# Kernel tuning notes

Measured on AMD Instinct MI355X. Metric: run time of the kernel, lower is better.

The kernel has to match this reference:

```python
import jax, jax.numpy as jnp
import numpy as np

N = 50000
E = 1000000
FN = 16
FE = 8
H = 64
DH = 64
LN_EPS = 1e-5


def _layernorm(x, g, b):
    mu = jnp.mean(x, axis=-1, keepdims=True)
    var = jnp.var(x, axis=-1, keepdims=True)
    return (x - mu) * jax.lax.rsqrt(var + LN_EPS) * g + b


def setup_inputs() -> dict:
    key = jax.random.key(0)
    ks = jax.random.split(key, 24)

    def w(k, i, o):
        return jax.random.normal(k, (i, o), jnp.float32) / np.sqrt(i).astype(np.float32)

    inp = {}
    inp["x"] = jax.random.normal(ks[0], (N, FN), jnp.float32)
    inp["edge_index"] = jax.random.randint(ks[1], (2, E), 0, N, dtype=jnp.int32)
    inp["edge_attr"] = jax.random.normal(ks[2], (E, FE), jnp.float32)
    # layer 0 (in_dim = FN, residual is a Linear since FN != H)
    inp["l0_lin_w"] = w(ks[3], FE, FN); inp["l0_lin_b"] = jnp.zeros((FN,), jnp.float32)
    inp["l0_w1"] = w(ks[4], FN, H);    inp["l0_b1"] = jnp.zeros((H,), jnp.float32)
    inp["l0_w2"] = w(ks[5], H, H);     inp["l0_b2"] = jnp.zeros((H,), jnp.float32)
    inp["l0_ln_g"] = jnp.ones((H,), jnp.float32); inp["l0_ln_b"] = jnp.zeros((H,), jnp.float32)
    inp["l0_res_w"] = w(ks[6], FN, H); inp["l0_res_b"] = jnp.zeros((H,), jnp.float32)
    # layers 1, 2 (in_dim = H, residual = identity)
    for li, base in ((1, 7), (2, 11)):
        inp[f"l{li}_lin_w"] = w(ks[base], FE, H);   inp[f"l{li}_lin_b"] = jnp.zeros((H,), jnp.float32)
        inp[f"l{li}_w1"] = w(ks[base + 1], H, H);   inp[f"l{li}_b1"] = jnp.zeros((H,), jnp.float32)
        inp[f"l{li}_w2"] = w(ks[base + 2], H, H);   inp[f"l{li}_b2"] = jnp.zeros((H,), jnp.float32)
        inp[f"l{li}_ln_g"] = jnp.ones((H,), jnp.float32)
        inp[f"l{li}_ln_b"] = jnp.zeros((H,), jnp.float32)
    D_IN = 4 * H + FE
    inp["dec_w1"] = w(ks[20], D_IN, DH);    inp["dec_b1"] = jnp.zeros((DH,), jnp.float32)
    inp["dec_w2"] = w(ks[21], DH, DH // 2); inp["dec_b2"] = jnp.zeros((DH // 2,), jnp.float32)
    inp["dec_w3"] = w(ks[22], DH // 2, 1);  inp["dec_b3"] = jnp.zeros((1,), jnp.float32)
    return inp


def _block(x, src, dst, edge_attr, lin_w, lin_b, w1, b1, w2, b2, ln_g, ln_b, res):
    # GINEConv: message = ReLU(x_src + Lin(edge_attr)); sum-aggregate at dst; eps=0
    msg = jax.nn.relu(x[src] + edge_attr @ lin_w + lin_b)      # (E, D_in)
    aggr = jax.ops.segment_sum(msg, dst, num_segments=N)       # (N, D_in)
    h = jax.nn.relu((x + aggr) @ w1 + b1) @ w2 + b2            # GIN nn MLP -> (N, H)
    h = jax.nn.relu(h)                                         # dropout inactive (eval)
    return _layernorm(h + res, ln_g, ln_b)


def reference(x, edge_index, edge_attr,
              l0_lin_w, l0_lin_b, l0_w1, l0_b1, l0_w2, l0_b2, l0_ln_g, l0_ln_b, l0_res_w, l0_res_b,
              l1_lin_w, l1_lin_b, l1_w1, l1_b1, l1_w2, l1_b2, l1_ln_g, l1_ln_b,
              l2_lin_w, l2_lin_b, l2_w1, l2_b1, l2_w2, l2_b2, l2_ln_g, l2_ln_b,
              dec_w1, dec_b1, dec_w2, dec_b2, dec_w3, dec_b3):
    src, dst = edge_index[0], edge_index[1]
    h = _block(x, src, dst, edge_attr, l0_lin_w, l0_lin_b, l0_w1, l0_b1, l0_w2, l0_b2,
               l0_ln_g, l0_ln_b, x @ l0_res_w + l0_res_b)
    h = _block(h, src, dst, edge_attr, l1_lin_w, l1_lin_b, l1_w1, l1_b1, l1_w2, l1_b2,
               l1_ln_g, l1_ln_b, h)
    h = _block(h, src, dst, edge_attr, l2_lin_w, l2_lin_b, l2_w1, l2_b1, l2_w2, l2_b2,
               l2_ln_g, l2_ln_b, h)
    hs, hd = h[src], h[dst]                                    # (E, H) each
    z = jnp.concatenate([hs, hd, jnp.abs(hs - hd), hs * hd, edge_attr], axis=-1)  # (E, 4H+FE)
    z = jax.nn.relu(z @ dec_w1 + dec_b1)
    z = jax.nn.relu(z @ dec_w2 + dec_b2)
    return (z @ dec_w3 + dec_b3)[:, 0]                         # (E,)
```

## Files before the change

kernel.cpp:

```cpp
#include <hip/hip_runtime.h>

#define NN 50000
#define NE 1000000

constexpr float LN_EPS = 1e-5f;

typedef short bf16x8 __attribute__((ext_vector_type(8)));
typedef float f32x4 __attribute__((ext_vector_type(4)));
typedef uint uvec4 __attribute__((ext_vector_type(4)));
typedef uint uvec2 __attribute__((ext_vector_type(2)));

__device__ inline uint cvtpk(float a, float b) {
  uint r;
  asm("v_cvt_pk_bf16_f32 %0, %1, %2" : "=v"(r) : "v"(a), "v"(b));
  return r;
}
__device__ inline ushort cvt1(float a) {
  uint r;
  asm("v_cvt_pk_bf16_f32 %0, %1, %1" : "=v"(r) : "v"(a));
  return (ushort)r;
}
__device__ inline float bflo(uint u) { union { uint x; float f; } v; v.x = u << 16; return v.f; }
__device__ inline float bfhi(uint u) { union { uint x; float f; } v; v.x = u & 0xffff0000u; return v.f; }

__global__ __launch_bounds__(256) void hist_kernel(const int* __restrict__ ei,
                                                   int* __restrict__ cnt) {
  int e = blockIdx.x * 256 + threadIdx.x;
  if (e < NE) atomicAdd(&cnt[ei[NE + e]], 1);
}

__global__ __launch_bounds__(256) void scan1_kernel(const int* __restrict__ cnt,
                                                    int* __restrict__ off,
                                                    int* __restrict__ bsum) {
  __shared__ int sh[256];
  int t = threadIdx.x;
  int idx = blockIdx.x * 256 + t;
  int v = (idx < NN) ? cnt[idx] : 0;
  sh[t] = v;
  __syncthreads();
  for (int o = 1; o < 256; o <<= 1) {
    int xv = (t >= o) ? sh[t - o] : 0;
    __syncthreads();
    sh[t] += xv;
    __syncthreads();
  }
  if (idx <= NN) off[idx] = sh[t] - v;
  if (t == 255) bsum[blockIdx.x] = sh[255];
}

__global__ __launch_bounds__(256) void scan2_kernel(int* __restrict__ bsum, int nb) {
  __shared__ int sh[256];
  int t = threadIdx.x;
  int v = (t < nb) ? bsum[t] : 0;
  sh[t] = v;
  __syncthreads();
  for (int o = 1; o < 256; o <<= 1) {
    int xv = (t >= o) ? sh[t - o] : 0;
    __syncthreads();
    sh[t] += xv;
    __syncthreads();
  }
  if (t < nb) bsum[t] = sh[t] - v;
}

__global__ __launch_bounds__(256) void scan3_kernel(int* __restrict__ off,
                                                    const int* __restrict__ bsum,
                                                    int* __restrict__ cnt) {
  int idx = blockIdx.x * 256 + threadIdx.x;
  if (idx <= NN) off[idx] += bsum[blockIdx.x];
  if (idx < NN) cnt[idx] = 0;
}

__global__ __launch_bounds__(256) void scatter_kernel(
    const int* __restrict__ ei, const float* __restrict__ ea,
    const int* __restrict__ off, int* __restrict__ cur,
    int* __restrict__ ipos, int* __restrict__ srcp, int* __restrict__ dstp,
    ushort* __restrict__ eapb) {
  int e = blockIdx.x * 256 + threadIdx.x;
  if (e < NE) {
    int d = ei[NE + e];
    int s = ei[e];
    int p = off[d] + atomicAdd(&cur[d], 1);
    ipos[e] = p;
    srcp[p] = s;
    dstp[p] = d;
    const float* eaf = ea + (size_t)e * 8;
    f32x4 e0 = *(const f32x4*)(eaf);
    f32x4 e1 = *(const f32x4*)(eaf + 4);
    uvec4 u;
    u.x = cvtpk(e0.x, e0.y);
    u.y = cvtpk(e0.z, e0.w);
    u.z = cvtpk(e1.x, e1.y);
    u.w = cvtpk(e1.z, e1.w);
    __builtin_nontemporal_store(u, (uvec4*)(eapb + (size_t)p * 8));
  }
}

__global__ __launch_bounds__(256) void unperm_kernel(const float* __restrict__ tmp,
                                                     const int* __restrict__ ipos,
                                                     float* __restrict__ out) {
  int e = blockIdx.x * 256 + threadIdx.x;
  if (e < NE) out[e] = tmp[ipos[e]];
}

__device__ inline float lane_layernorm(float r, float g, float b) {
  float s = r;
#pragma unroll
  for (int m = 32; m >= 1; m >>= 1) s += __shfl_xor(s, m);
  float mu = s * (1.f / 64.f);
  float dv = r - mu;
  float v = dv * dv;
#pragma unroll
  for (int m = 32; m >= 1; m >>= 1) v += __shfl_xor(v, m);
  float var = v * (1.f / 64.f);
  return dv * rsqrtf(var + LN_EPS) * g + b;
}

__global__ __launch_bounds__(256) void layer0_fused(
    const float* __restrict__ x, float* __restrict__ hout,
    ushort* __restrict__ houtbf,
    const ushort* __restrict__ eapb, const int* __restrict__ srcp,
    const int* __restrict__ off,
    const float* __restrict__ lw, const float* __restrict__ lb,
    const float* __restrict__ w1, const float* __restrict__ b1,
    const float* __restrict__ w2, const float* __restrict__ b2,
    const float* __restrict__ lng, const float* __restrict__ lnb,
    const float* __restrict__ rw, const float* __restrict__ rb) {
  int n = blockIdx.x * 4 + (threadIdx.x >> 6);
  int j = threadIdx.x & 63;
  int d = j & 15, slot = j >> 4;
  int start = off[n], end = off[n + 1];
  float lwv[8];
#pragma unroll
  for (int i = 0; i < 8; i++) lwv[i] = lw[i * 16 + d];
  float lbv = lb[d];
  float acc = 0.f;
  for (int base = start; base < end; base += 64) {
    int idx = base + j;
    int sl = (idx < end) ? srcp[idx] : 0;
    int c = min(end - base, 64);
    for (int i0 = 0; i0 < c; i0 += 4) {
      int i = i0 + slot;
      bool valid = i < c;
      int ii = i & 63;
      int s = __shfl(sl, ii);
      int pp = min(base + i0 + slot, NE - 1);
      float ev = bflo((uint)eapb[(size_t)pp * 8 + (d & 7)]);
      float xs = x[(size_t)s * 16 + d];
      float m = lbv + xs;
#pragma unroll
      for (int q = 0; q < 8; q++) m = fmaf(__shfl(ev, slot * 16 + q), lwv[q], m);
      m = fmaxf(m, 0.f);
      acc += valid ? m : 0.f;
    }
  }
  acc += __shfl_xor(acc, 16);
  acc += __shfl_xor(acc, 32);
  float xr = x[(size_t)n * 16 + d];
  float t = xr + acc;
  float q1 = b1[j];
#pragma unroll 4
  for (int k = 0; k < 16; k++) q1 = fmaf(__shfl(t, k), w1[k * 64 + j], q1);
  q1 = fmaxf(q1, 0.f);
  float h2 = b2[j];
  for (int k = 0; k < 64; k++) h2 = fmaf(__shfl(q1, k), w2[k * 64 + j], h2);
  h2 = fmaxf(h2, 0.f);
  float res = rb[j];
#pragma unroll 4
  for (int k = 0; k < 16; k++) res = fmaf(__shfl(xr, k), rw[k * 64 + j], res);
  float v = lane_layernorm(h2 + res, lng[j], lnb[j]);
  hout[(size_t)n * 64 + j] = v;
  houtbf[(size_t)n * 64 + j] = cvt1(v);
}

__device__ inline float edge8_msg(const ushort* __restrict__ hinb, int s, int j,
                                  uint ulo, uint uhi, uint vlo, uint vhi,
                                  const float* lwv, float lbv) {
  float hc = bflo((uint)hinb[(size_t)s * 64 + j]);
  float m = lbv + hc;
  m = fmaf(bflo(ulo), lwv[0], m);
  m = fmaf(bfhi(ulo), lwv[1], m);
  m = fmaf(bflo(uhi), lwv[2], m);
  m = fmaf(bfhi(uhi), lwv[3], m);
  m = fmaf(bflo(vlo), lwv[4], m);
  m = fmaf(bfhi(vlo), lwv[5], m);
  m = fmaf(bflo(vhi), lwv[6], m);
  m = fmaf(bfhi(vhi), lwv[7], m);
  return fmaxf(m, 0.f);
}

__global__ __launch_bounds__(256) void aggr_kernel(
    const ushort* __restrict__ hinb, float* __restrict__ tout,
    const ushort* __restrict__ eapb, const int* __restrict__ srcp,
    const int* __restrict__ off,
    const float* __restrict__ lw, const float* __restrict__ lb) {
  int n = blockIdx.x * 4 + (threadIdx.x >> 6);
  int j = threadIdx.x & 63;
  int start = __builtin_amdgcn_readfirstlane(off[n]);
  int end = __builtin_amdgcn_readfirstlane(off[n + 1]);
  float lwv[8];
#pragma unroll
  for (int i = 0; i < 8; i++) lwv[i] = lw[i * 64 + j];
  float lbv = lb[j];
  float acc = 0.f;
  int p = start;
  for (; p + 8 <= end; p += 8) {
    const uvec4* ip = (const uvec4*)(srcp + p);
    uvec4 I0 = __builtin_nontemporal_load(ip + 0);
    uvec4 I1 = __builtin_nontemporal_load(ip + 1);
    int s0 = __builtin_amdgcn_readfirstlane((int)I0.x);
    int s1 = __builtin_amdgcn_readfirstlane((int)I0.y);
    int s2 = __builtin_amdgcn_readfirstlane((int)I0.z);
    int s3 = __builtin_amdgcn_readfirstlane((int)I0.w);
    int s4 = __builtin_amdgcn_readfirstlane((int)I1.x);
    int s5 = __builtin_amdgcn_readfirstlane((int)I1.y);
    int s6 = __builtin_amdgcn_readfirstlane((int)I1.z);
    int s7 = __builtin_amdgcn_readfirstlane((int)I1.w);
    const uvec4* ep = (const uvec4*)(eapb + (size_t)p * 8);
    uint ua[8][4];
#pragma unroll
    for (int i = 0; i < 8; i++) {
      uvec4 E = __builtin_nontemporal_load(ep + i);
      ua[i][0] = __builtin_amdgcn_readfirstlane(E.x);
      ua[i][1] = __builtin_amdgcn_readfirstlane(E.y);
      ua[i][2] = __builtin_amdgcn_readfirstlane(E.z);
      ua[i][3] = __builtin_amdgcn_readfirstlane(E.w);
    }
    acc += edge8_msg(hinb, s0, j, ua[0][0], ua[0][1], ua[0][2], ua[0][3], lwv, lbv);
    acc += edge8_msg(hinb, s1, j, ua[1][0], ua[1][1], ua[1][2], ua[1][3], lwv, lbv);
    acc += edge8_msg(hinb, s2, j, ua[2][0], ua[2][1], ua[2][2], ua[2][3], lwv, lbv);
    acc += edge8_msg(hinb, s3, j, ua[3][0], ua[3][1], ua[3][2], ua[3][3], lwv, lbv);
    acc += edge8_msg(hinb, s4, j, ua[4][0], ua[4][1], ua[4][2], ua[4][3], lwv, lbv);
    acc += edge8_msg(hinb, s5, j, ua[5][0], ua[5][1], ua[5][2], ua[5][3], lwv, lbv);
    acc += edge8_msg(hinb, s6, j, ua[6][0], ua[6][1], ua[6][2], ua[6][3], lwv, lbv);
    acc += edge8_msg(hinb, s7, j, ua[7][0], ua[7][1], ua[7][2], ua[7][3], lwv, lbv);
  }
  for (; p < end; p++) {
    int s = __builtin_amdgcn_readfirstlane(srcp[p]);
    uvec4 E = __builtin_nontemporal_load((const uvec4*)(eapb + (size_t)p * 8));
    uint e0 = __builtin_amdgcn_readfirstlane(E.x);
    uint e1 = __builtin_amdgcn_readfirstlane(E.y);
    uint e2 = __builtin_amdgcn_readfirstlane(E.z);
    uint e3 = __builtin_amdgcn_readfirstlane(E.w);
    acc += edge8_msg(hinb, s, j, e0, e1, e2, e3, lwv, lbv);
  }
  tout[(size_t)n * 64 + j] = acc;
}

__global__ __launch_bounds__(256) void prep_kernel(
    const float* __restrict__ w1, const float* __restrict__ w2,
    ushort* __restrict__ w1f, ushort* __restrict__ w2f) {
  int t = blockIdx.x * 256 + threadIdx.x;
  if (t < 18432) {
    int j = t & 7, lane = (t >> 3) & 63, f = t >> 9;
    int k = (f >> 2) * 32 + ((lane >> 4) * 8) + j;
    int n = (f & 3) * 16 + (lane & 15);
    float v = (k < 264) ? w1[k * 64 + n] : 0.f;
    w1f[t] = cvt1(v);
  } else {
    int t2 = t - 18432;
    int j = t2 & 7, lane = (t2 >> 3) & 63, f = t2 >> 9;
    int k = (f >> 1) * 32 + ((lane >> 4) * 8) + j;
    int n = (f & 1) * 16 + (lane & 15);
    w2f[t2] = cvt1(w2[k * 32 + n]);
  }
}

__global__ __launch_bounds__(256) void prep_mlpw(
    const float* __restrict__ w1a, const float* __restrict__ w2a,
    const float* __restrict__ w1b, const float* __restrict__ w2b,
    ushort* __restrict__ out) {
  int t = blockIdx.x * 256 + threadIdx.x;
  int layer = t >> 13, wsel = (t >> 12) & 1, idx = t & 4095;
  const float* w = layer ? (wsel ? w2b : w1b) : (wsel ? w2a : w1a);
  int j = idx & 7, lane = (idx >> 3) & 63, f = idx >> 9;
  int k = (f >> 2) * 32 + ((lane >> 4) * 8) + j;
  int n = (f & 3) * 16 + (lane & 15);
  float v = w[k * 64 + n];
  ushort h = cvt1(v);
  float r = v - bflo((uint)h);
  ushort lo = cvt1(r);
  int base = layer * 16384 + wsel * 8192;
  out[base + idx] = h;
  out[base + 4096 + idx] = lo;
}

#define YS2 68

__global__ __launch_bounds__(128) void mlp_kernel(
    const float* __restrict__ tacc, const float* __restrict__ hinf,
    float* __restrict__ houtf, ushort* __restrict__ houtbf,
    const ushort* __restrict__ wf,
    const float* __restrict__ b1, const float* __restrict__ b2,
    const float* __restrict__ lng, const float* __restrict__ lnb) {
  __shared__ float ybuf[2][32 * YS2];
  const int w = threadIdx.x >> 6, l = threadIdx.x & 63;
  const int sub = l & 15, quad = l >> 4;
  const int wid = blockIdx.x * 2 + w;
  const int r0 = wid * 32;
  if (r0 >= NN) return;
  float* Y = ybuf[w];

  const bf16x8* w1h = (const bf16x8*)wf;
  const bf16x8* w1l = (const bf16x8*)(wf + 4096);
  const bf16x8* w2h = (const bf16x8*)(wf + 8192);
  const bf16x8* w2l = (const bf16x8*)(wf + 12288);

  union UF { uvec4 u; bf16x8 v; };

  bf16x8 Ahi[2][2], Alo[2][2];
#pragma unroll
  for (int m = 0; m < 2; m++) {
    int row = min(r0 + m * 16 + sub, NN - 1);
    const float* pt = tacc + (size_t)row * 64 + quad * 8;
    const float* ph = hinf + (size_t)row * 64 + quad * 8;
#pragma unroll
    for (int ks = 0; ks < 2; ks++) {
      f32x4 t0 = *(const f32x4*)(pt + ks * 32);
      f32x4 t1 = *(const f32x4*)(pt + ks * 32 + 4);
      f32x4 h0 = *(const f32x4*)(ph + ks * 32);
      f32x4 h1 = *(const f32x4*)(ph + ks * 32 + 4);
      t0 += h0;
      t1 += h1;
      UF uh, ul;
      uh.u.x = cvtpk(t0.x, t0.y);
      uh.u.y = cvtpk(t0.z, t0.w);
      uh.u.z = cvtpk(t1.x, t1.y);
      uh.u.w = cvtpk(t1.z, t1.w);
      ul.u.x = cvtpk(t0.x - bflo(uh.u.x), t0.y - bfhi(uh.u.x));
      ul.u.y = cvtpk(t0.z - bflo(uh.u.y), t0.w - bfhi(uh.u.y));
      ul.u.z = cvtpk(t1.x - bflo(uh.u.z), t1.y - bfhi(uh.u.z));
      ul.u.w = cvtpk(t1.z - bflo(uh.u.w), t1.w - bfhi(uh.u.w));
      Ahi[m][ks] = uh.v;
      Alo[m][ks] = ul.v;
    }
  }

  f32x4 c1[2][4];
#pragma unroll
  for (int m = 0; m < 2; m++)
#pragma unroll
    for (int nb = 0; nb < 4; nb++) c1[m][nb] = (f32x4){0.f, 0.f, 0.f, 0.f};
#pragma unroll
  for (int nb = 0; nb < 4; nb++) {
#pragma unroll
    for (int ks = 0; ks < 2; ks++) {
      bf16x8 bh = w1h[(ks * 4 + nb) * 64 + l];
      bf16x8 bl = w1l[(ks * 4 + nb) * 64 + l];
      c1[0][nb] = __builtin_amdgcn_mfma_f32_16x16x32_bf16(Ahi[0][ks], bh, c1[0][nb], 0, 0, 0);
      c1[1][nb] = __builtin_amdgcn_mfma_f32_16x16x32_bf16(Ahi[1][ks], bh, c1[1][nb], 0, 0, 0);
      c1[0][nb] = __builtin_amdgcn_mfma_f32_16x16x32_bf16(Alo[0][ks], bh, c1[0][nb], 0, 0, 0);
      c1[1][nb] = __builtin_amdgcn_mfma_f32_16x16x32_bf16(Alo[1][ks], bh, c1[1][nb], 0, 0, 0);
      c1[0][nb] = __builtin_amdgcn_mfma_f32_16x16x32_bf16(Ahi[0][ks], bl, c1[0][nb], 0, 0, 0);
      c1[1][nb] = __builtin_amdgcn_mfma_f32_16x16x32_bf16(Ahi[1][ks], bl, c1[1][nb], 0, 0, 0);
    }
  }

  float b1v[4];
#pragma unroll
  for (int nb = 0; nb < 4; nb++) b1v[nb] = b1[nb * 16 + sub];
#pragma unroll
  for (int m = 0; m < 2; m++)
#pragma unroll
    for (int nb = 0; nb < 4; nb++)
#pragma unroll
      for (int r = 0; r < 4; r++)
        Y[(m * 16 + quad * 4 + r) * YS2 + nb * 16 + sub] =
            fmaxf(c1[m][nb][r] + b1v[nb], 0.f);

  bf16x8 Qhi[2][2], Qlo[2][2];
#pragma unroll
  for (int m = 0; m < 2; m++) {
#pragma unroll
    for (int ks = 0; ks < 2; ks++) {
      const float* py = &Y[(m * 16 + sub) * YS2 + ks * 32 + quad * 8];
      f32x4 q0 = *(const f32x4*)py;
      f32x4 q1 = *(const f32x4*)(py + 4);
      UF uh, ul;
      uh.u.x = cvtpk(q0.x, q0.y);
      uh.u.y = cvtpk(q0.z, q0.w);
      uh.u.z = cvtpk(q1.x, q1.y);
      uh.u.w = cvtpk(q1.z, q1.w);
      ul.u.x = cvtpk(q0.x - bflo(uh.u.x), q0.y - bfhi(uh.u.x));
      ul.u.y = cvtpk(q0.z - bflo(uh.u.y), q0.w - bfhi(uh.u.y));
      ul.u.z = cvtpk(q1.x - bflo(uh.u.z), q1.y - bfhi(uh.u.z));
      ul.u.w = cvtpk(q1.z - bflo(uh.u.w), q1.w - bfhi(uh.u.w));
      Qhi[m][ks] = uh.v;
      Qlo[m][ks] = ul.v;
    }
  }

  f32x4 c2[2][4];
#pragma unroll
  for (int m = 0; m < 2; m++)
#pragma unroll
    for (int nb = 0; nb < 4; nb++) c2[m][nb] = (f32x4){0.f, 0.f, 0.f, 0.f};
#pragma unroll
  for (int nb = 0; nb < 4; nb++) {
#pragma unroll
    for (int ks = 0; ks < 2; ks++) {
      bf16x8 bh = w2h[(ks * 4 + nb) * 64 + l];
      bf16x8 bl = w2l[(ks * 4 + nb) * 64 + l];
      c2[0][nb] = __builtin_amdgcn_mfma_f32_16x16x32_bf16(Qhi[0][ks], bh, c2[0][nb], 0, 0, 0);
      c2[1][nb] = __builtin_amdgcn_mfma_f32_16x16x32_bf16(Qhi[1][ks], bh, c2[1][nb], 0, 0, 0);
      c2[0][nb] = __builtin_amdgcn_mfma_f32_16x16x32_bf16(Qlo[0][ks], bh, c2[0][nb], 0, 0, 0);
      c2[1][nb] = __builtin_amdgcn_mfma_f32_16x16x32_bf16(Qlo[1][ks], bh, c2[1][nb], 0, 0, 0);
      c2[0][nb] = __builtin_amdgcn_mfma_f32_16x16x32_bf16(Qhi[0][ks], bl, c2[0][nb], 0, 0, 0);
      c2[1][nb] = __builtin_amdgcn_mfma_f32_16x16x32_bf16(Qhi[1][ks], bl, c2[1][nb], 0, 0, 0);
    }
  }

  float b2v[4], lngv[4], lnbv[4];
#pragma unroll
  for (int nb = 0; nb < 4; nb++) {
    b2v[nb] = b2[nb * 16 + sub];
    lngv[nb] = lng[nb * 16 + sub];
    lnbv[nb] = lnb[nb * 16 + sub];
  }
#pragma unroll
  for (int m = 0; m < 2; m++) {
#pragma unroll
    for (int r = 0; r < 4; r++) {
      int node = r0 + m * 16 + quad * 4 + r;
      int nc = min(node, NN - 1);
      float vp[4];
      float s = 0.f;
#pragma unroll
      for (int nb = 0; nb < 4; nb++) {
        vp[nb] = fmaxf(c2[m][nb][r] + b2v[nb], 0.f) +
                 hinf[(size_t)nc * 64 + nb * 16 + sub];
        s += vp[nb];
      }
      s += __shfl_xor(s, 1);
      s += __shfl_xor(s, 2);
      s += __shfl_xor(s, 4);
      s += __shfl_xor(s, 8);
      float mu = s * (1.f / 64.f);
      float vv = 0.f;
      float dv[4];
#pragma unroll
      for (int nb = 0; nb < 4; nb++) {
        dv[nb] = vp[nb] - mu;
        vv += dv[nb] * dv[nb];
      }
      vv += __shfl_xor(vv, 1);
      vv += __shfl_xor(vv, 2);
      vv += __shfl_xor(vv, 4);
      vv += __shfl_xor(vv, 8);
      float rstd = rsqrtf(vv * (1.f / 64.f) + LN_EPS);
      if (node < NN) {
#pragma unroll
        for (int nb = 0; nb < 4; nb++) {
          float o = dv[nb] * rstd * lngv[nb] + lnbv[nb];
          if (houtf) houtf[(size_t)node * 64 + nb * 16 + sub] = o;
          houtbf[(size_t)node * 64 + nb * 16 + sub] = cvt1(o);
        }
      }
    }
  }
}

#define YS 72
#define NBLK 15625
#define BPX 1954

__device__ inline void absmul(bf16x8 a, bf16x8 b, bf16x8& dd, bf16x8& pp) {
  union U { bf16x8 v; uvec4 u; } ua, ub, ud, up;
  ua.v = a; ub.v = b;
#pragma unroll
  for (int i = 0; i < 4; i++) {
    float a0 = bflo(ua.u[i]), a1 = bfhi(ua.u[i]);
    float b0 = bflo(ub.u[i]), b1 = bfhi(ub.u[i]);
    ud.u[i] = cvtpk(fabsf(a0 - b0), fabsf(a1 - b1));
    up.u[i] = cvtpk(a0 * b0, a1 * b1);
  }
  dd = ud.v; pp = up.v;
}

__global__ __launch_bounds__(128, 4) void decoder_kernel(
    const ushort* __restrict__ hb,
    const int* __restrict__ srcp, const int* __restrict__ dstp,
    const ushort* __restrict__ eapb,
    const ushort* __restrict__ w1f, const ushort* __restrict__ w2f,
    const float* __restrict__ b1, const float* __restrict__ b2,
    const float* __restrict__ w3, const float* __restrict__ b3,
    float* __restrict__ tmp) {
  __shared__ ushort ybuf[2][32 * YS];
  const int w = threadIdx.x >> 6, l = threadIdx.x & 63;
  const int sub = l & 15, quad = l >> 4;
  int bb = (blockIdx.x & 7) * BPX + (blockIdx.x >> 3);
  if (bb >= NBLK) return;
  const int g = bb * 2 + w;
  ushort* Y = ybuf[w];

  int s32 = __builtin_nontemporal_load(&srcp[g * 32 + (l & 31)]);
  int d32 = __builtin_nontemporal_load(&dstp[g * 32 + (l & 31)]);

  bf16x8 alo[2], ahi[2], blo[2], bhi[2];
#pragma unroll
  for (int m = 0; m < 2; m++) {
    int sA = __shfl(s32, m * 16 + sub);
    int dA = __shfl(d32, m * 16 + sub);
    const ushort* pa = hb + (size_t)sA * 64 + quad * 8;
    const ushort* pb = hb + (size_t)dA * 64 + quad * 8;
    alo[m] = *(const bf16x8*)pa;
    ahi[m] = *(const bf16x8*)(pa + 32);
    blo[m] = *(const bf16x8*)pb;
    bhi[m] = *(const bf16x8*)(pb + 32);
  }
  bf16x8 eaf0 = (bf16x8){0, 0, 0, 0, 0, 0, 0, 0};
  bf16x8 eaf1 = (bf16x8){0, 0, 0, 0, 0, 0, 0, 0};
  if (quad == 0) {
    eaf0 = *(const bf16x8*)&eapb[((size_t)g * 32 + sub) * 8];
    eaf1 = *(const bf16x8*)&eapb[((size_t)g * 32 + 16 + sub) * 8];
  }

  float b1v[4];
#pragma unroll
  for (int t = 0; t < 4; t++) b1v[t] = b1[t * 16 + sub];
  float b2v0 = b2[sub], b2v1 = b2[16 + sub];
  float w3v0 = w3[sub], w3v1 = w3[16 + sub];
  float b3v = b3[0];

  f32x4 acc[2][4];
#pragma unroll
  for (int m = 0; m < 2; m++)
#pragma unroll
    for (int t = 0; t < 4; t++) acc[m][t] = (f32x4){0.f, 0.f, 0.f, 0.f};

#define MF(sB, f0, f1)                                                        \
  {                                                                           \
    _Pragma("unroll") for (int t = 0; t < 4; t++) {                           \
      bf16x8 bfv = ((const bf16x8*)w1f)[((sB)*4 + t) * 64 + l];               \
      acc[0][t] = __builtin_amdgcn_mfma_f32_16x16x32_bf16(f0, bfv, acc[0][t], \
                                                          0, 0, 0);           \
      acc[1][t] = __builtin_amdgcn_mfma_f32_16x16x32_bf16(f1, bfv, acc[1][t], \
                                                          0, 0, 0);           \
    }                                                                         \
  }

  {
    bf16x8 dlo0, plo0, dlo1, plo1;
    absmul(alo[0], blo[0], dlo0, plo0);
    absmul(alo[1], blo[1], dlo1, plo1);
    MF(0, alo[0], alo[1]);
    MF(2, blo[0], blo[1]);
    MF(4, dlo0, dlo1);
    MF(6, plo0, plo1);
  }
  {
    bf16x8 dhi0, phi0, dhi1, phi1;
    absmul(ahi[0], bhi[0], dhi0, phi0);
    absmul(ahi[1], bhi[1], dhi1, phi1);
    MF(1, ahi[0], ahi[1]);
    MF(3, bhi[0], bhi[1]);
    MF(5, dhi0, dhi1);
    MF(7, phi0, phi1);
  }
  MF(8, eaf0, eaf1);
#undef MF

#pragma unroll
  for (int m = 0; m < 2; m++)
#pragma unroll
    for (int t = 0; t < 4; t++)
#pragma unroll
      for (int r = 0; r < 4; r++)
        Y[(m * 16 + quad * 4 + r) * YS + t * 16 + sub] =
            cvt1(fmaxf(acc[m][t][r] + b1v[t], 0.f));

  bf16x8 w2frag[4];
#pragma unroll
  for (int f = 0; f < 4; f++) w2frag[f] = ((const bf16x8*)w2f)[f * 64 + l];
  f32x4 acc2[2][2];
#pragma unroll
  for (int m = 0; m < 2; m++) {
    acc2[m][0] = (f32x4){0.f, 0.f, 0.f, 0.f};
    acc2[m][1] = (f32x4){0.f, 0.f, 0.f, 0.f};
#pragma unroll
    for (int ks = 0; ks < 2; ks++) {
      bf16x8 ya = *(const bf16x8*)&Y[(m * 16 + sub) * YS + ks * 32 + quad * 8];
      acc2[m][0] = __builtin_amdgcn_mfma_f32_16x16x32_bf16(ya, w2frag[ks * 2 + 0],
                                                           acc2[m][0], 0, 0, 0);
      acc2[m][1] = __builtin_amdgcn_mfma_f32_16x16x32_bf16(ya, w2frag[ks * 2 + 1],
                                                           acc2[m][1], 0, 0, 0);
    }
  }
#pragma unroll
  for (int m = 0; m < 2; m++)
#pragma unroll
    for (int r = 0; r < 4; r++) {
      float o = fmaxf(acc2[m][0][r] + b2v0, 0.f) * w3v0 +
                fmaxf(acc2[m][1][r] + b2v1, 0.f) * w3v1;
      o += __shfl_xor(o, 1);
      o += __shfl_xor(o, 2);
      o += __shfl_xor(o, 4);
      o += __shfl_xor(o, 8);
      if (sub == 0) tmp[g * 32 + m * 16 + quad * 4 + r] = o + b3v;
    }
}

extern "C" void kernel_launch(void* const* d_in, const int* in_sizes, int n_in,
                              void* d_out, int out_size, void* d_ws, size_t ws_size,
                              hipStream_t stream) {
  const float* x = (const float*)d_in[0];
  const int* ei = (const int*)d_in[1];
  const float* ea = (const float*)d_in[2];
  const float* l0_lin_w = (const float*)d_in[3];
  const float* l0_lin_b = (const float*)d_in[4];
  const float* l0_w1 = (const float*)d_in[5];
  const float* l0_b1 = (const float*)d_in[6];
  const float* l0_w2 = (const float*)d_in[7];
  const float* l0_b2 = (const float*)d_in[8];
  const float* l0_ln_g = (const float*)d_in[9];
  const float* l0_ln_b = (const float*)d_in[10];
  const float* l0_res_w = (const float*)d_in[11];
  const float* l0_res_b = (const float*)d_in[12];
  const float* dec_w1 = (const float*)d_in[29];
  const float* dec_b1 = (const float*)d_in[30];
  const float* dec_w2 = (const float*)d_in[31];
  const float* dec_b2 = (const float*)d_in[32];
  const float* dec_w3 = (const float*)d_in[33];
  const float* dec_b3 = (const float*)d_in[34];

  float* h_a = (float*)d_ws;
  float* h_b = h_a + (size_t)NN * 64;
  ushort* hbA = (ushort*)(h_b + (size_t)NN * 64);
  ushort* hbB = hbA + (size_t)NN * 64;
  int* ipos = (int*)(hbB + (size_t)NN * 64);
  int* srcp = ipos + NE;
  int* dstp = srcp + NE;
  float* tmp = (float*)(dstp + NE);
  int* off = (int*)(tmp + NE);
  int* cnt = off + (NN + 1);
  int* bsum = cnt + NN;
  ushort* w1f = (ushort*)(bsum + 256);
  ushort* w2f = w1f + 18432;
  ushort* eapb = w2f + 2048;
  ushort* wmlp = eapb + (size_t)NE * 8;
  float* tacc = (float*)(wmlp + 32768);

  const int EB = (NE + 255) / 256;
  const int SB = (NN + 256) / 256;
  const int MB = ((NN + 31) / 32 + 1) / 2;

  hipMemsetAsync(cnt, 0, (size_t)NN * sizeof(int), stream);
  hist_kernel<<<EB, 256, 0, stream>>>(ei, cnt);
  scan1_kernel<<<SB, 256, 0, stream>>>(cnt, off, bsum);
  scan2_kernel<<<1, 256, 0, stream>>>(bsum, SB);
  scan3_kernel<<<SB, 256, 0, stream>>>(off, bsum, cnt);
  scatter_kernel<<<EB, 256, 0, stream>>>(ei, ea, off, cnt, ipos, srcp, dstp, eapb);
  prep_mlpw<<<64, 256, 0, stream>>>((const float*)d_in[15], (const float*)d_in[17],
                                    (const float*)d_in[23], (const float*)d_in[25],
                                    wmlp);

  layer0_fused<<<NN / 4, 256, 0, stream>>>(x, h_a, hbA, eapb, srcp, off,
                                           l0_lin_w, l0_lin_b, l0_w1, l0_b1,
                                           l0_w2, l0_b2, l0_ln_g, l0_ln_b,
                                           l0_res_w, l0_res_b);
  aggr_kernel<<<NN / 4, 256, 0, stream>>>(hbA, tacc, eapb, srcp, off,
                                          (const float*)d_in[13],
                                          (const float*)d_in[14]);
  mlp_kernel<<<MB, 128, 0, stream>>>(tacc, h_a, h_b, hbB, wmlp,
                                     (const float*)d_in[16], (const float*)d_in[18],
                                     (const float*)d_in[19], (const float*)d_in[20]);
  aggr_kernel<<<NN / 4, 256, 0, stream>>>(hbB, tacc, eapb, srcp, off,
                                          (const float*)d_in[21],
                                          (const float*)d_in[22]);
  mlp_kernel<<<MB, 128, 0, stream>>>(tacc, h_b, (float*)nullptr, hbA, wmlp + 16384,
                                     (const float*)d_in[24], (const float*)d_in[26],
                                     (const float*)d_in[27], (const float*)d_in[28]);

  prep_kernel<<<80, 256, 0, stream>>>(dec_w1, dec_w2, w1f, w2f);
  decoder_kernel<<<8 * BPX, 128, 0, stream>>>(hbA, srcp, dstp, eapb,
                                              w1f, w2f, dec_b1, dec_b2,
                                              dec_w3, dec_b3, tmp);
  unperm_kernel<<<EB, 256, 0, stream>>>(tmp, ipos, (float*)d_out);
}
```

Before: 572.6 us.

## Split layer-0 into aggregation and MFMA-based node MLP kernels

The fused layer-0 kernel, which ran its node MLP with per-lane scalar FMA loops over shuffles, is split in two. An aggregation kernel now writes 16-wide aggregated sums, and a new mlp0 kernel computes W1, W2 and the residual projection with bf16 split-precision (hi/lo) MFMA plus layernorm, using pre-packed weights. This moves the dense per-node work off slow shuffle-FMA loops, at the cost of an extra launch and a round trip of the 16-wide sums through global memory.

```diff
diff --git a/kernel.cpp b/kernel.cpp
--- a/kernel.cpp
+++ b/kernel.cpp
@@ -103,29 +103,11 @@
   if (e < NE) out[e] = tmp[ipos[e]];
 }
 
-__device__ inline float lane_layernorm(float r, float g, float b) {
-  float s = r;
-#pragma unroll
-  for (int m = 32; m >= 1; m >>= 1) s += __shfl_xor(s, m);
-  float mu = s * (1.f / 64.f);
-  float dv = r - mu;
-  float v = dv * dv;
-#pragma unroll
-  for (int m = 32; m >= 1; m >>= 1) v += __shfl_xor(v, m);
-  float var = v * (1.f / 64.f);
-  return dv * rsqrtf(var + LN_EPS) * g + b;
-}
-
-__global__ __launch_bounds__(256) void layer0_fused(
-    const float* __restrict__ x, float* __restrict__ hout,
-    ushort* __restrict__ houtbf,
+__global__ __launch_bounds__(256) void aggr0_kernel(
+    const float* __restrict__ x, float* __restrict__ tout16,
     const ushort* __restrict__ eapb, const int* __restrict__ srcp,
     const int* __restrict__ off,
-    const float* __restrict__ lw, const float* __restrict__ lb,
-    const float* __restrict__ w1, const float* __restrict__ b1,
-    const float* __restrict__ w2, const float* __restrict__ b2,
-    const float* __restrict__ lng, const float* __restrict__ lnb,
-    const float* __restrict__ rw, const float* __restrict__ rb) {
+    const float* __restrict__ lw, const float* __restrict__ lb) {
   int n = blockIdx.x * 4 + (threadIdx.x >> 6);
   int j = threadIdx.x & 63;
   int d = j & 15, slot = j >> 4;
@@ -156,21 +138,7 @@
   }
   acc += __shfl_xor(acc, 16);
   acc += __shfl_xor(acc, 32);
-  float xr = x[(size_t)n * 16 + d];
-  float t = xr + acc;
-  float q1 = b1[j];
-#pragma unroll 4
-  for (int k = 0; k < 16; k++) q1 = fmaf(__shfl(t, k), w1[k * 64 + j], q1);
-  q1 = fmaxf(q1, 0.f);
-  float h2 = b2[j];
-  for (int k = 0; k < 64; k++) h2 = fmaf(__shfl(q1, k), w2[k * 64 + j], h2);
-  h2 = fmaxf(h2, 0.f);
-  float res = rb[j];
-#pragma unroll 4
-  for (int k = 0; k < 16; k++) res = fmaf(__shfl(xr, k), rw[k * 64 + j], res);
-  float v = lane_layernorm(h2 + res, lng[j], lnb[j]);
-  hout[(size_t)n * 64 + j] = v;
-  houtbf[(size_t)n * 64 + j] = cvt1(v);
+  if (slot == 0) tout16[(size_t)n * 16 + d] = acc;
 }
 
 __device__ inline float edge8_msg(const ushort* __restrict__ hinb, int s, int j,
@@ -285,6 +253,36 @@
   out[base + 4096 + idx] = lo;
 }
 
+__global__ __launch_bounds__(256) void prep_mlp0(
+    const float* __restrict__ w1, const float* __restrict__ w2,
+    const float* __restrict__ rw, ushort* __restrict__ out) {
+  int t = blockIdx.x * 256 + threadIdx.x;
+  if (t < 4096) {
+    int which = t >> 11, idx = t & 2047;
+    int j = idx & 7, lane = (idx >> 3) & 63, f = idx >> 9;
+    int k = ((lane >> 4) * 8) + j;
+    int n = f * 16 + (lane & 15);
+    float v;
+    if (which == 0) v = (k < 16) ? w1[k * 64 + n] : 0.f;
+    else            v = (k >= 16) ? rw[(k - 16) * 64 + n] : 0.f;
+    ushort h = cvt1(v);
+    float r = v - bflo((uint)h);
+    int base = which * 4096;
+    out[base + idx] = h;
+    out[base + 2048 + idx] = cvt1(r);
+  } else {
+    int idx = t - 4096;
+    int j = idx & 7, lane = (idx >> 3) & 63, f = idx >> 9;
+    int k = (f >> 2) * 32 + ((lane >> 4) * 8) + j;
+    int n = (f & 3) * 16 + (lane & 15);
+    float v = w2[k * 64 + n];
+    ushort h = cvt1(v);
+    float r = v - bflo((uint)h);
+    out[8192 + idx] = h;
+    out[12288 + idx] = cvt1(r);
+  }
+}
+
 #define YS2 68
 
 __global__ __launch_bounds__(128) void mlp_kernel(
@@ -453,6 +451,186 @@
         for (int nb = 0; nb < 4; nb++) {
           float o = dv[nb] * rstd * lngv[nb] + lnbv[nb];
           if (houtf) houtf[(size_t)node * 64 + nb * 16 + sub] = o;
+          houtbf[(size_t)node * 64 + nb * 16 + sub] = cvt1(o);
+        }
+      }
+    }
+  }
+}
+
+__global__ __launch_bounds__(128) void mlp0_kernel(
+    const float* __restrict__ x, const float* __restrict__ tacc16,
+    float* __restrict__ houtf, ushort* __restrict__ houtbf,
+    const ushort* __restrict__ wf,
+    const float* __restrict__ b1, const float* __restrict__ b2,
+    const float* __restrict__ rb,
+    const float* __restrict__ lng, const float* __restrict__ lnb) {
+  __shared__ float ybuf[2][32 * YS2];
+  const int w = threadIdx.x >> 6, l = threadIdx.x & 63;
+  const int sub = l & 15, quad = l >> 4;
+  const int wid = blockIdx.x * 2 + w;
+  const int r0 = wid * 32;
+  if (r0 >= NN) return;
+  float* Y = ybuf[w];
+
+  const bf16x8* B1h = (const bf16x8*)wf;
+  const bf16x8* B1l = (const bf16x8*)(wf + 2048);
+  const bf16x8* B2h = (const bf16x8*)(wf + 4096);
+  const bf16x8* B2l = (const bf16x8*)(wf + 6144);
+  const bf16x8* W2h = (const bf16x8*)(wf + 8192);
+  const bf16x8* W2l = (const bf16x8*)(wf + 12288);
+
+  union UF { uvec4 u; bf16x8 v; };
+
+  bf16x8 Ahi[2], Alo[2];
+#pragma unroll
+  for (int m = 0; m < 2; m++) {
+    int row = min(r0 + m * 16 + sub, NN - 1);
+    const float* px = x + (size_t)row * 16 + (quad & 1) * 8;
+    f32x4 v0 = *(const f32x4*)px;
+    f32x4 v1 = *(const f32x4*)(px + 4);
+    if (quad < 2) {
+      const float* pt = tacc16 + (size_t)row * 16 + (quad & 1) * 8;
+      v0 += *(const f32x4*)pt;
+      v1 += *(const f32x4*)(pt + 4);
+    }
+    UF uh, ul;
+    uh.u.x = cvtpk(v0.x, v0.y);
+    uh.u.y = cvtpk(v0.z, v0.w);
+    uh.u.z = cvtpk(v1.x, v1.y);
+    uh.u.w = cvtpk(v1.z, v1.w);
+    ul.u.x = cvtpk(v0.x - bflo(uh.u.x), v0.y - bfhi(uh.u.x));
+    ul.u.y = cvtpk(v0.z - bflo(uh.u.y), v0.w - bfhi(uh.u.y));
+    ul.u.z = cvtpk(v1.x - bflo(uh.u.z), v1.y - bfhi(uh.u.z));
+    ul.u.w = cvtpk(v1.z - bflo(uh.u.w), v1.w - bfhi(uh.u.w));
+    Ahi[m] = uh.v;
+    Alo[m] = ul.v;
+  }
+
+  f32x4 c1[2][4], cr[2][4];
+#pragma unroll
+  for (int m = 0; m < 2; m++)
+#pragma unroll
+    for (int nb = 0; nb < 4; nb++) {
+      c1[m][nb] = (f32x4){0.f, 0.f, 0.f, 0.f};
+      cr[m][nb] = (f32x4){0.f, 0.f, 0.f, 0.f};
+    }
+#pragma unroll
+  for (int nb = 0; nb < 4; nb++) {
+    bf16x8 bh = B1h[nb * 64 + l];
+    bf16x8 bl = B1l[nb * 64 + l];
+    c1[0][nb] = __builtin_amdgcn_mfma_f32_16x16x32_bf16(Ahi[0], bh, c1[0][nb], 0, 0, 0);
+    c1[1][nb] = __builtin_amdgcn_mfma_f32_16x16x32_bf16(Ahi[1], bh, c1[1][nb], 0, 0, 0);
+    c1[0][nb] = __builtin_amdgcn_mfma_f32_16x16x32_bf16(Alo[0], bh, c1[0][nb], 0, 0, 0);
+    c1[1][nb] = __builtin_amdgcn_mfma_f32_16x16x32_bf16(Alo[1], bh, c1[1][nb], 0, 0, 0);
+    c1[0][nb] = __builtin_amdgcn_mfma_f32_16x16x32_bf16(Ahi[0], bl, c1[0][nb], 0, 0, 0);
+    c1[1][nb] = __builtin_amdgcn_mfma_f32_16x16x32_bf16(Ahi[1], bl, c1[1][nb], 0, 0, 0);
+    bf16x8 rh = B2h[nb * 64 + l];
+    bf16x8 rl = B2l[nb * 64 + l];
+    cr[0][nb] = __builtin_amdgcn_mfma_f32_16x16x32_bf16(Ahi[0], rh, cr[0][nb], 0, 0, 0);
+    cr[1][nb] = __builtin_amdgcn_mfma_f32_16x16x32_bf16(Ahi[1], rh, cr[1][nb], 0, 0, 0);
+    cr[0][nb] = __builtin_amdgcn_mfma_f32_16x16x32_bf16(Alo[0], rh, cr[0][nb], 0, 0, 0);
+    cr[1][nb] = __builtin_amdgcn_mfma_f32_16x16x32_bf16(Alo[1], rh, cr[1][nb], 0, 0, 0);
+    cr[0][nb] = __builtin_amdgcn_mfma_f32_16x16x32_bf16(Ahi[0], rl, cr[0][nb], 0, 0, 0);
+    cr[1][nb] = __builtin_amdgcn_mfma_f32_16x16x32_bf16(Ahi[1], rl, cr[1][nb], 0, 0, 0);
+  }
+
+  float b1v[4];
+#pragma unroll
+  for (int nb = 0; nb < 4; nb++) b1v[nb] = b1[nb * 16 + sub];
+#pragma unroll
+  for (int m = 0; m < 2; m++)
+#pragma unroll
+    for (int nb = 0; nb < 4; nb++)
+#pragma unroll
+      for (int r = 0; r < 4; r++)
+        Y[(m * 16 + quad * 4 + r) * YS2 + nb * 16 + sub] =
+            fmaxf(c1[m][nb][r] + b1v[nb], 0.f);
+
+  bf16x8 Qhi[2][2], Qlo[2][2];
+#pragma unroll
+  for (int m = 0; m < 2; m++) {
+#pragma unroll
+    for (int ks = 0; ks < 2; ks++) {
+      const float* py = &Y[(m * 16 + sub) * YS2 + ks * 32 + quad * 8];
+      f32x4 q0 = *(const f32x4*)py;
+      f32x4 q1 = *(const f32x4*)(py + 4);
+      UF uh, ul;
+      uh.u.x = cvtpk(q0.x, q0.y);
+      uh.u.y = cvtpk(q0.z, q0.w);
+      uh.u.z = cvtpk(q1.x, q1.y);
+      uh.u.w = cvtpk(q1.z, q1.w);
+      ul.u.x = cvtpk(q0.x - bflo(uh.u.x), q0.y - bfhi(uh.u.x));
+      ul.u.y = cvtpk(q0.z - bflo(uh.u.y), q0.w - bfhi(uh.u.y));
+      ul.u.z = cvtpk(q1.x - bflo(uh.u.z), q1.y - bfhi(uh.u.z));
+      ul.u.w = cvtpk(q1.z - bflo(uh.u.w), q1.w - bfhi(uh.u.w));
+      Qhi[m][ks] = uh.v;
+      Qlo[m][ks] = ul.v;
+    }
+  }
+
+  f32x4 c2[2][4];
+#pragma unroll
+  for (int m = 0; m < 2; m++)
+#pragma unroll
+    for (int nb = 0; nb < 4; nb++) c2[m][nb] = (f32x4){0.f, 0.f, 0.f, 0.f};
+#pragma unroll
+  for (int nb = 0; nb < 4; nb++) {
+#pragma unroll
+    for (int ks = 0; ks < 2; ks++) {
+      bf16x8 bh = W2h[(ks * 4 + nb) * 64 + l];
+      bf16x8 bl = W2l[(ks * 4 + nb) * 64 + l];
+      c2[0][nb] = __builtin_amdgcn_mfma_f32_16x16x32_bf16(Qhi[0][ks], bh, c2[0][nb], 0, 0, 0);
+      c2[1][nb] = __builtin_amdgcn_mfma_f32_16x16x32_bf16(Qhi[1][ks], bh, c2[1][nb], 0, 0, 0);
+      c2[0][nb] = __builtin_amdgcn_mfma_f32_16x16x32_bf16(Qlo[0][ks], bh, c2[0][nb], 0, 0, 0);
+      c2[1][nb] = __builtin_amdgcn_mfma_f32_16x16x32_bf16(Qlo[1][ks], bh, c2[1][nb], 0, 0, 0);
+      c2[0][nb] = __builtin_amdgcn_mfma_f32_16x16x32_bf16(Qhi[0][ks], bl, c2[0][nb], 0, 0, 0);
+      c2[1][nb] = __builtin_amdgcn_mfma_f32_16x16x32_bf16(Qhi[1][ks], bl, c2[1][nb], 0, 0, 0);
+    }
+  }
+
+  float b2v[4], rbv[4], lngv[4], lnbv[4];
+#pragma unroll
+  for (int nb = 0; nb < 4; nb++) {
+    b2v[nb] = b2[nb * 16 + sub];
+    rbv[nb] = rb[nb * 16 + sub];
+    lngv[nb] = lng[nb * 16 + sub];
+    lnbv[nb] = lnb[nb * 16 + sub];
+  }
+#pragma unroll
+  for (int m = 0; m < 2; m++) {
+#pragma unroll
+    for (int r = 0; r < 4; r++) {
+      int node = r0 + m * 16 + quad * 4 + r;
+      float vp[4];
+      float s = 0.f;
+#pragma unroll
+      for (int nb = 0; nb < 4; nb++) {
+        vp[nb] = fmaxf(c2[m][nb][r] + b2v[nb], 0.f) + cr[m][nb][r] + rbv[nb];
+        s += vp[nb];
+      }
+      s += __shfl_xor(s, 1);
+      s += __shfl_xor(s, 2);
+      s += __shfl_xor(s, 4);
+      s += __shfl_xor(s, 8);
+      float mu = s * (1.f / 64.f);
+      float vv = 0.f;
+      float dv[4];
+#pragma unroll
+      for (int nb = 0; nb < 4; nb++) {
+        dv[nb] = vp[nb] - mu;
+        vv += dv[nb] * dv[nb];
+      }
+      vv += __shfl_xor(vv, 1);
+      vv += __shfl_xor(vv, 2);
+      vv += __shfl_xor(vv, 4);
+      vv += __shfl_xor(vv, 8);
+      float rstd = rsqrtf(vv * (1.f / 64.f) + LN_EPS);
+      if (node < NN) {
+#pragma unroll
+        for (int nb = 0; nb < 4; nb++) {
+          float o = dv[nb] * rstd * lngv[nb] + lnbv[nb];
+          houtf[(size_t)node * 64 + nb * 16 + sub] = o;
           houtbf[(size_t)node * 64 + nb * 16 + sub] = cvt1(o);
         }
       }
@@ -638,7 +816,8 @@
   ushort* w2f = w1f + 18432;
   ushort* eapb = w2f + 2048;
   ushort* wmlp = eapb + (size_t)NE * 8;
-  float* tacc = (float*)(wmlp + 32768);
+  ushort* wmlp0 = wmlp + 32768;
+  float* tacc = (float*)(wmlp0 + 16384);
 
   const int EB = (NE + 255) / 256;
   const int SB = (NN + 256) / 256;
@@ -653,11 +832,13 @@
   prep_mlpw<<<64, 256, 0, stream>>>((const float*)d_in[15], (const float*)d_in[17],
                                     (const float*)d_in[23], (const float*)d_in[25],
                                     wmlp);
-
-  layer0_fused<<<NN / 4, 256, 0, stream>>>(x, h_a, hbA, eapb, srcp, off,
-                                           l0_lin_w, l0_lin_b, l0_w1, l0_b1,
-                                           l0_w2, l0_b2, l0_ln_g, l0_ln_b,
-                                           l0_res_w, l0_res_b);
+  prep_mlp0<<<32, 256, 0, stream>>>(l0_w1, l0_w2, l0_res_w, wmlp0);
+
+  aggr0_kernel<<<NN / 4, 256, 0, stream>>>(x, tacc, eapb, srcp, off,
+                                           l0_lin_w, l0_lin_b);
+  mlp0_kernel<<<MB, 128, 0, stream>>>(x, tacc, h_a, hbA, wmlp0,
+                                      l0_b1, l0_b2, l0_res_b, l0_ln_g, l0_ln_b);
+
   aggr_kernel<<<NN / 4, 256, 0, stream>>>(hbA, tacc, eapb, srcp, off,
                                           (const float*)d_in[13],
                                           (const float*)d_in[14]);
```

After: 543.8 us. -5.0%, faster.
